# Optimization experiments

Hardware: AMD Instinct MI355X
Metric: run time of the kernel (lower is better)

## Reference

```python
import jax, jax.numpy as jnp
import numpy as np

V = 200      # v_dim
H = 400      # hidden
B, N = 1024, 128


def setup_inputs() -> dict:
    key = jax.random.key(0)
    ks = jax.random.split(key, 32)
    rn = lambda k, s, sc=0.05: jax.random.normal(k, s, dtype=jnp.float32) * sc
    merged = rn(ks[0], (B, N, 15), 1.0)
    # last column is the active flag in {0,1}; subject row (row 0) is active
    flag = jax.random.randint(ks[1], (B, N), 0, 2).astype(jnp.float32)
    flag = flag.at[:, 0].set(1.0)
    merged = merged.at[:, :, 14].set(flag)
    x = rn(ks[2], (B, N, 8), 1.0)
    a = rn(ks[3], (B,), 1.0)
    p = {
        # aug_attention = CrossAttentionLayer(7, 14, 200)
        'Wq_aug': rn(ks[4], (7, V)),  'bq_aug': rn(ks[5], (V,)),
        'Wk_aug': rn(ks[6], (14, V)), 'bk_aug': rn(ks[7], (V,)),
        'Wv_aug': rn(ks[8], (14, V)), 'bv_aug': rn(ks[9], (V,)),
        # o_attention = CrossAttentionLayer(7, 7, 200)
        'Wq_o': rn(ks[10], (7, V)),  'bq_o': rn(ks[11], (V,)),
        'Wk_o': rn(ks[12], (7, V)), 'bk_o': rn(ks[13], (V,)),
        'Wv_o': rn(ks[14], (7, V)), 'bv_o': rn(ks[15], (V,)),
        # shared BatchNorm1d(200)
        'bn_g': jnp.ones((V,), jnp.float32), 'bn_b': jnp.zeros((V,), jnp.float32),
        # six 200->200->1 ELU heads stacked: order [u,u_,d,d_,o,o_]
        'W3': rn(ks[16], (6, V, 200)), 'b3': rn(ks[17], (6, 200)),
        'W4': rn(ks[18], (6, 200)),    'b4': rn(ks[19], (6,)),
        # ego critic MLP 4->400->400->1
        'W0': rn(ks[20], (4, H)), 'b0': rn(ks[21], (H,)),
        'W1': rn(ks[22], (H, H)), 'b1': rn(ks[23], (H,)),
        'W2': rn(ks[24], (H, 1)), 'b2': rn(ks[25], (1,)),
    }
    return {'merged': merged, 'x': x, 'a': a, **p}


def _forward(merged, x, a, Wq_aug, bq_aug, Wk_aug, bk_aug, Wv_aug, bv_aug,
             Wq_o, bq_o, Wk_o, bk_o, Wv_o, bv_o, bn_g, bn_b,
             W3, b3, W4, b4, W0, b0, W1, b1, W2, b2):
    # --- event critic preprocessing (relative bus index) ---
    sub_bus = merged[:, 0, 0]
    merged = merged.at[:, :, 0].add(-sub_bus[:, None])
    merged = merged.at[:, :, 7].add(-sub_bus[:, None])
    sub_loc = merged[:, 0, 2][:, None]        # subject location
    flag = merged[:, :, 14]
    loc = merged[:, :, 2]
    u_mask = (loc < sub_loc) & (flag == 1.0)
    d_mask = (loc > sub_loc) & (flag == 1.0)
    f0 = flag == 0.0
    o_mask = f0 & (jnp.cumsum(f0.astype(jnp.int32), axis=1) > 1)  # drop first flag==0 row ([1:])
    ego7 = merged[:, 0, :7]                    # [B,7]
    scale = 1.0 / np.sqrt(float(V))

    def attend(Wq, bq, Wk, bk, Wv, bv, kv, masks):
        # variable-length cross-attention as masked softmax over padded keys
        q = ego7 @ Wq + bq                            # [B,V]
        k = jnp.einsum('bnf,fd->bnd', kv, Wk) + bk    # [B,N,V]
        v = jnp.einsum('bnf,fd->bnd', kv, Wv) + bv    # [B,N,V]
        s = jnp.einsum('bd,bnd->bn', q, k) * scale    # [B,N]
        outs = []
        for m in masks:
            w = jax.nn.softmax(jnp.where(m, s, -1e9), axis=1)
            o = jnp.einsum('bn,bnd->bd', w, v)
            outs.append(jnp.where(m.any(axis=1, keepdims=True), o, 0.0))
        return outs

    u_t, d_t = attend(Wq_aug, bq_aug, Wk_aug, bk_aug, Wv_aug, bv_aug,
                      merged[:, :, :14], [u_mask, d_mask])
    (o_t,) = attend(Wq_o, bq_o, Wk_o, bk_o, Wv_o, bv_o,
                    merged[:, :, :7], [o_mask])

    def bn(t):  # BatchNorm1d in training mode: per-call batch stats (biased var)
        m = t.mean(axis=0)
        var = t.var(axis=0)
        return bn_g * (t - m) / jnp.sqrt(var + 1e-5) + bn_b

    t = jnp.stack([bn(u_t), bn(d_t), bn(o_t)], axis=1)   # [B,3,V]
    th = t[:, jnp.array([0, 0, 1, 1, 2, 2])]             # [B,6,V] heads [u,u_,d,d_,o,o_]
    h = jax.nn.elu(jnp.einsum('bkf,kfg->bkg', th, W3) + b3)
    heads = jnp.einsum('bkg,kg->bk', h, W4) + b4         # [B,6]
    A1 = (heads[:, 0] + heads[:, 2] + heads[:, 4])[:, None]
    A2 = (heads[:, 1] + heads[:, 3] + heads[:, 5])[:, None]

    # --- ego critic ---
    ego4 = jnp.concatenate([x[:, 0, 4:7], a[:, None]], axis=1)  # cols [4,5,6], last <- a
    h1 = jax.nn.relu(ego4 @ W0 + b0)
    h1 = jax.nn.relu(h1 @ W1 + b1)
    Q1 = h1 @ W2 + b2                                    # [B,1]

    G1 = (Q1 + A1).reshape(-1, 1)
    G2 = (Q1 + A2).reshape(-1, 1)
    reg = jnp.zeros((1,), jnp.float32)
    return Q1, A2, G1, G2, reg


def reference(merged, x, a, Wq_aug, bq_aug, Wk_aug, bk_aug, Wv_aug, bv_aug,
              Wq_o, bq_o, Wk_o, bk_o, Wv_o, bv_o, bn_g, bn_b,
              W3, b3, W4, b4, W0, b0, W1, b1, W2, b2):
    return _forward(merged, x, a, Wq_aug, bq_aug, Wk_aug, bk_aug, Wv_aug, bv_aug,
                    Wq_o, bq_o, Wk_o, bk_o, Wv_o, bv_o, bn_g, bn_b,
                    W3, b3, W4, b4, W0, b0, W1, b1, W2, b2)
```

## Files before the change

kernel.cpp:

```cpp
#include <hip/hip_runtime.h>

#define BB 1024
#define NN 128
#define VV 200
#define HH 400

__device__ inline float wave_sum(float v){
  for (int o=32;o>0;o>>=1) v += __shfl_down(v,o);
  return v;
}
__device__ inline float xsum(float v){
  for (int o=1;o<64;o<<=1) v += __shfl_xor(v,o);
  return v;
}
__device__ inline float xmax(float v){
  for (int o=1;o<64;o<<=1) v = fmaxf(v,__shfl_xor(v,o));
  return v;
}

__global__ __launch_bounds__(64) void prep_k(
    const float* __restrict__ Wq_aug, const float* __restrict__ bq_aug,
    const float* __restrict__ Wk_aug, const float* __restrict__ bk_aug,
    const float* __restrict__ Wq_o,  const float* __restrict__ bq_o,
    const float* __restrict__ Wk_o,  const float* __restrict__ bk_o,
    float* __restrict__ prep)
{
  int t = blockIdx.x;
  int lane = threadIdx.x;
  const float *A, *Bv;
  if (t<98)      { int i=t/14, f=t-i*14; A=Wq_aug+i*VV; Bv=Wk_aug+f*VV; }
  else if (t<112){ int f=t-98;           A=bq_aug;      Bv=Wk_aug+f*VV; }
  else if (t<119){ int i=t-112;          A=Wq_aug+i*VV; Bv=bk_aug; }
  else if (t==119){                      A=bq_aug;      Bv=bk_aug; }
  else if (t<169){ int r=t-120; int i=r/7, f=r-i*7; A=Wq_o+i*VV; Bv=Wk_o+f*VV; }
  else if (t<176){ int f=t-169;          A=bq_o;        Bv=Wk_o+f*VV; }
  else if (t<183){ int i=t-176;          A=Wq_o+i*VV;   Bv=bk_o; }
  else           {                       A=bq_o;        Bv=bk_o; }
  float s=0;
  for (int d=lane; d<VV; d+=64) s += A[d]*Bv[d];
  s = xsum(s);
  if (lane==0) prep[t]=s;
}

__global__ __launch_bounds__(64) void attn_v2(
    const float* __restrict__ merged, const float* __restrict__ prep,
    const float* __restrict__ Wv_aug, const float* __restrict__ bv_aug,
    const float* __restrict__ Wv_o,  const float* __restrict__ bv_o,
    float* __restrict__ t_buf)
{
  const int b = blockIdx.x;
  const int lane = threadIdx.x;
  const float* base = merged + (size_t)b*NN*15;

  float sub_bus = base[0], sub_loc = base[2];
  float eg[7];
  eg[0]=0.0f;
  for (int i=1;i<7;i++) eg[i]=base[i];

  float wkqa[14], wkqo[7];
  #pragma unroll
  for (int f=0;f<14;f++){
    float s = prep[98+f];
    for (int i=1;i<7;i++) s += eg[i]*prep[i*14+f];
    wkqa[f]=s;
  }
  float qbka = prep[119];
  for (int i=1;i<7;i++) qbka += eg[i]*prep[112+i];
  #pragma unroll
  for (int f=0;f<7;f++){
    float s = prep[169+f];
    for (int i=1;i<7;i++) s += eg[i]*prep[120+i*7+f];
    wkqo[f]=s;
  }
  float qbko = prep[183];
  for (int i=1;i<7;i++) qbko += eg[i]*prep[176+i];

  float m0[15], m1[15];
  const float* r0 = base + (size_t)lane*15;
  const float* r1 = base + (size_t)(lane+64)*15;
  #pragma unroll
  for (int i=0;i<15;i++){ m0[i]=r0[i]; m1[i]=r1[i]; }
  m0[0]-=sub_bus; m0[7]-=sub_bus;
  m1[0]-=sub_bus; m1[7]-=sub_bus;

  const float scale = 0.07071067811865475f;
  float sa0=qbka, sa1=qbka, so0=qbko, so1=qbko;
  #pragma unroll
  for (int f=0;f<14;f++){ sa0+=m0[f]*wkqa[f]; sa1+=m1[f]*wkqa[f]; }
  #pragma unroll
  for (int f=0;f<7;f++){ so0+=m0[f]*wkqo[f]; so1+=m1[f]*wkqo[f]; }
  sa0*=scale; sa1*=scale; so0*=scale; so1*=scale;

  float fl0=m0[14], fl1=m1[14], lo0=m0[2], lo1=m1[2];
  bool um0=(lo0<sub_loc)&&(fl0==1.0f), um1=(lo1<sub_loc)&&(fl1==1.0f);
  bool dm0=(lo0>sub_loc)&&(fl0==1.0f), dm1=(lo1>sub_loc)&&(fl1==1.0f);
  bool f00=(fl0==0.0f), f01=(fl1==0.0f);
  unsigned long long bal0=__ballot(f00), bal1=__ballot(f01);
  unsigned long long below=(1ull<<lane)-1ull;
  int prior0=__popcll(bal0&below);
  int prior1=__popcll(bal0)+__popcll(bal1&below);
  bool om0=f00&&(prior0>0), om1=f01&&(prior1>0);

  const float NINF=-3.0e38f;
  float mu_ = xmax(fmaxf(um0?sa0:NINF, um1?sa1:NINF));
  bool anyu = mu_>-1e38f;
  float eu0 = um0?expf(sa0-mu_):0.0f, eu1 = um1?expf(sa1-mu_):0.0f;
  float su = xsum(eu0+eu1);
  float ivu = anyu?1.0f/su:0.0f;
  float wu0=eu0*ivu, wu1=eu1*ivu;
  float md_ = xmax(fmaxf(dm0?sa0:NINF, dm1?sa1:NINF));
  bool anyd = md_>-1e38f;
  float ed0 = dm0?expf(sa0-md_):0.0f, ed1 = dm1?expf(sa1-md_):0.0f;
  float sd = xsum(ed0+ed1);
  float ivd = anyd?1.0f/sd:0.0f;
  float wd0=ed0*ivd, wd1=ed1*ivd;
  float mo_ = xmax(fmaxf(om0?so0:NINF, om1?so1:NINF));
  bool anyo = mo_>-1e38f;
  float eo0 = om0?expf(so0-mo_):0.0f, eo1 = om1?expf(so1-mo_):0.0f;
  float so = xsum(eo0+eo1);
  float ivo = anyo?1.0f/so:0.0f;
  float wo0=eo0*ivo, wo1=eo1*ivo;

  float wfu[14], wfd[14], wfo[7];
  #pragma unroll
  for (int f=0;f<14;f++){
    wfu[f]=xsum(wu0*m0[f]+wu1*m1[f]);
    wfd[f]=xsum(wd0*m0[f]+wd1*m1[f]);
  }
  #pragma unroll
  for (int f=0;f<7;f++) wfo[f]=xsum(wo0*m0[f]+wo1*m1[f]);

  float* tb = t_buf + (size_t)b*600;
  #pragma unroll
  for (int rep=0;rep<4;rep++){
    int c = lane + rep*64;
    if (c < VV){
      float uv=bv_aug[c], dv=bv_aug[c], ov=bv_o[c];
      #pragma unroll
      for (int f=0;f<14;f++){
        float w=Wv_aug[f*VV+c];
        uv+=wfu[f]*w; dv+=wfd[f]*w;
      }
      #pragma unroll
      for (int f=0;f<7;f++) ov+=wfo[f]*Wv_o[f*VV+c];
      if(!anyu) uv=0.0f;
      if(!anyd) dv=0.0f;
      if(!anyo) ov=0.0f;
      tb[c]=uv; tb[200+c]=dv; tb[400+c]=ov;
    }
  }
}

__global__ __launch_bounds__(256) void bn_mlp(
    const float* __restrict__ t_buf,
    float* __restrict__ mean_out, float* __restrict__ rstd_out,
    const float* __restrict__ x, const float* __restrict__ a,
    const float* __restrict__ W0, const float* __restrict__ b0,
    const float* __restrict__ W1, const float* __restrict__ b1,
    const float* __restrict__ W2,
    float* __restrict__ mlp_part)
{
  int tid=threadIdx.x, wv=tid>>6, lane=tid&63;
  __shared__ float smem[8*HH + 4*64*9 + 64];

  if (blockIdx.x < 150){
    int c0 = blockIdx.x*4;
    float* ls  = smem;
    float* ls2 = smem+16;
    float s[4]={0,0,0,0}, s2[4]={0,0,0,0};
    #pragma unroll 2
    for (int b=tid;b<BB;b+=256){
      float4 v = *reinterpret_cast<const float4*>(t_buf + (size_t)b*600 + c0);
      s[0]+=v.x; s[1]+=v.y; s[2]+=v.z; s[3]+=v.w;
      s2[0]+=v.x*v.x; s2[1]+=v.y*v.y; s2[2]+=v.z*v.z; s2[3]+=v.w*v.w;
    }
    for (int c=0;c<4;c++){ s[c]=wave_sum(s[c]); s2[c]=wave_sum(s2[c]); }
    if (lane==0){
      for (int c=0;c<4;c++){ ls[wv*4+c]=s[c]; ls2[wv*4+c]=s2[c]; }
    }
    __syncthreads();
    if (tid<4){
      float S =ls[0*4+tid]+ls[1*4+tid]+ls[2*4+tid]+ls[3*4+tid];
      float S2=ls2[0*4+tid]+ls2[1*4+tid]+ls2[2*4+tid]+ls2[3*4+tid];
      float mean = S*(1.0f/BB);
      float var  = S2*(1.0f/BB) - mean*mean;
      mean_out[c0+tid]=mean;
      rstd_out[c0+tid]=rsqrtf(var+1e-5f);
    }
  } else {
    unsigned mu = blockIdx.x - 150;
    int js = mu >> 7;
    int xg = mu & 127;
    int bb = xg*8;
    float* h1s  = smem;
    float* part = smem + 8*HH;
    float* ego  = smem + 8*HH + 4*64*9;
    if (tid<32){
      int bl=tid>>2, j=tid&3;
      int b=bb+bl;
      ego[bl*4+j] = (j<3) ? x[(size_t)b*NN*8 + 4 + j] : a[b];
    }
    __syncthreads();
    for (int idx=tid; idx<8*HH; idx+=256){
      int bl = idx/HH, i = idx - bl*HH;
      float v = b0[i] + ego[bl*4+0]*W0[i]      + ego[bl*4+1]*W0[HH+i]
                      + ego[bl*4+2]*W0[2*HH+i] + ego[bl*4+3]*W0[3*HH+i];
      h1s[bl*HH+i] = fmaxf(v,0.0f);
    }
    __syncthreads();
    int jl = tid & 63;
    int ic = tid >> 6;
    int j  = js*64 + jl;
    bool jok = (j < HH);
    int jc = jok ? j : (HH-1);
    float acc[8]={0,0,0,0,0,0,0,0};
    {
      const float* w1p = W1 + jc;
      int i0 = ic*100;
      #pragma unroll 4
      for (int i=i0;i<i0+100;i++){
        float w = w1p[(size_t)i*HH];
        acc[0]+=h1s[0*HH+i]*w; acc[1]+=h1s[1*HH+i]*w;
        acc[2]+=h1s[2*HH+i]*w; acc[3]+=h1s[3*HH+i]*w;
        acc[4]+=h1s[4*HH+i]*w; acc[5]+=h1s[5*HH+i]*w;
        acc[6]+=h1s[6*HH+i]*w; acc[7]+=h1s[7*HH+i]*w;
      }
    }
    for (int bl=0;bl<8;bl++) part[(ic*64+jl)*9+bl]=acc[bl];
    __syncthreads();
    if (tid < 64){
      float bj = b1[jc], w2 = W2[jc];
      for (int bl=0;bl<8;bl++){
        float s = part[(0*64+jl)*9+bl]+part[(1*64+jl)*9+bl]
                + part[(2*64+jl)*9+bl]+part[(3*64+jl)*9+bl];
        s += bj;
        float contrib = jok ? fmaxf(s,0.0f)*w2 : 0.0f;
        float tot = wave_sum(contrib);
        if (jl==0) mlp_part[(size_t)(bb+bl)*8 + js] = tot;
      }
    }
  }
}

__global__ __launch_bounds__(256) void heads_k(
    const float* __restrict__ t_buf, const float* __restrict__ mean_in,
    const float* __restrict__ rstd_in,
    const float* __restrict__ bn_g, const float* __restrict__ bn_b,
    const float* __restrict__ W3, const float* __restrict__ b3,
    const float* __restrict__ W4, const float* __restrict__ b4,
    float* __restrict__ headv_ws)
{
  int bb = blockIdx.x*8;
  int k  = blockIdx.y;
  int tid=threadIdx.x, wv=tid>>6, lane=tid&63;
  int t3 = k>>1;
  __shared__ float tn[8][200];
  for (int idx=tid; idx<1600; idx+=256){
    int bl=idx/200, v=idx-bl*200;
    int c = t3*200+v;
    tn[bl][v] = bn_g[v]*(t_buf[(size_t)(bb+bl)*600+c]-mean_in[c])*rstd_in[c]+bn_b[v];
  }
  __syncthreads();
  float contrib[8]={0,0,0,0,0,0,0,0};
  int g = tid;
  if (g < 200){
    float acc[8];
    float bias = b3[k*200+g];
    for (int bl=0;bl<8;bl++) acc[bl]=bias;
    const float* w3p = W3 + (size_t)k*40000 + g;
    #pragma unroll 4
    for (int v=0;v<200;v++){
      float w = w3p[(size_t)v*200];
      acc[0]+=tn[0][v]*w; acc[1]+=tn[1][v]*w;
      acc[2]+=tn[2][v]*w; acc[3]+=tn[3][v]*w;
      acc[4]+=tn[4][v]*w; acc[5]+=tn[5][v]*w;
      acc[6]+=tn[6][v]*w; acc[7]+=tn[7][v]*w;
    }
    float w4 = W4[k*200+g];
    for (int bl=0;bl<8;bl++){
      float h = acc[bl]>0.f ? acc[bl] : (expf(acc[bl])-1.0f);
      contrib[bl] = h*w4;
    }
  }
  for (int bl=0;bl<8;bl++) contrib[bl]=wave_sum(contrib[bl]);
  __shared__ float red[4][8];
  if (lane==0) for (int bl=0;bl<8;bl++) red[wv][bl]=contrib[bl];
  __syncthreads();
  if (tid<8){
    float s = red[0][tid]+red[1][tid]+red[2][tid]+red[3][tid];
    headv_ws[(size_t)(bb+tid)*6 + k] = s + b4[k];
  }
}

__global__ __launch_bounds__(256) void finalize(
    const float* __restrict__ mlp_part, const float* __restrict__ headv_ws,
    const float* __restrict__ b2, float* __restrict__ out)
{
  int b = blockIdx.x*256 + threadIdx.x;
  if (b < BB){
    const float* mp = mlp_part + (size_t)b*8;
    float q = mp[0]+mp[1]+mp[2]+mp[3]+mp[4]+mp[5]+mp[6] + b2[0];
    const float* hv = headv_ws + (size_t)b*6;
    float A1 = hv[0]+hv[2]+hv[4];
    float A2 = hv[1]+hv[3]+hv[5];
    out[b]      = q;
    out[BB+b]   = A2;
    out[2*BB+b] = q+A1;
    out[3*BB+b] = q+A2;
    if (b==0) out[4*BB]=0.0f;
  }
}

extern "C" void kernel_launch(void* const* d_in, const int* in_sizes, int n_in,
                              void* d_out, int out_size, void* d_ws, size_t ws_size,
                              hipStream_t stream)
{
  (void)in_sizes; (void)n_in; (void)out_size; (void)ws_size;
  const float* merged=(const float*)d_in[0];
  const float* x     =(const float*)d_in[1];
  const float* a     =(const float*)d_in[2];
  const float* Wq_aug=(const float*)d_in[3];  const float* bq_aug=(const float*)d_in[4];
  const float* Wk_aug=(const float*)d_in[5];  const float* bk_aug=(const float*)d_in[6];
  const float* Wv_aug=(const float*)d_in[7];  const float* bv_aug=(const float*)d_in[8];
  const float* Wq_o  =(const float*)d_in[9];  const float* bq_o  =(const float*)d_in[10];
  const float* Wk_o  =(const float*)d_in[11]; const float* bk_o  =(const float*)d_in[12];
  const float* Wv_o  =(const float*)d_in[13]; const float* bv_o  =(const float*)d_in[14];
  const float* bn_g  =(const float*)d_in[15]; const float* bn_b  =(const float*)d_in[16];
  const float* W3    =(const float*)d_in[17]; const float* b3    =(const float*)d_in[18];
  const float* W4    =(const float*)d_in[19]; const float* b4    =(const float*)d_in[20];
  const float* W0    =(const float*)d_in[21]; const float* b0    =(const float*)d_in[22];
  const float* W1    =(const float*)d_in[23]; const float* b1    =(const float*)d_in[24];
  const float* W2    =(const float*)d_in[25]; const float* b2    =(const float*)d_in[26];

  float* out = (float*)d_out;
  float* ws  = (float*)d_ws;
  float* t_buf   = ws;
  float* mean_b  = ws + 614400;
  float* rstd_b  = ws + 615000;
  float* mlp_part= ws + 615600;
  float* headv_ws= ws + 623792;
  float* prep_b  = ws + 629936;

  hipLaunchKernelGGL(prep_k, dim3(184), dim3(64), 0, stream,
      Wq_aug,bq_aug,Wk_aug,bk_aug, Wq_o,bq_o,Wk_o,bk_o, prep_b);
  hipLaunchKernelGGL(attn_v2, dim3(BB), dim3(64), 0, stream,
      merged, prep_b, Wv_aug, bv_aug, Wv_o, bv_o, t_buf);
  hipLaunchKernelGGL(bn_mlp, dim3(150+896), dim3(256), 0, stream,
      t_buf, mean_b, rstd_b, x, a, W0, b0, W1, b1, W2, mlp_part);
  hipLaunchKernelGGL(heads_k, dim3(BB/8,6), dim3(256), 0, stream,
      t_buf, mean_b, rstd_b, bn_g, bn_b, W3, b3, W4, b4, headv_ws);
  hipLaunchKernelGGL(finalize, dim3(4), dim3(256), 0, stream,
      mlp_part, headv_ws, b2, out);
}
```

Measured before the change: 60.97 us.

## Fuse prep, attention, BN statistics and MLP into one front kernel

Merges the prep, attention and BN-stats/MLP kernels into a single `front` kernel. Each attention block now recomputes the 184 query-key dot products into shared memory and handles 4 batch rows, one per wave. Block-local channel sums and sums of squares are pushed into global fixed-point int64 atomics, which removes the separate BN reduction pass over t_buf. The heads kernel derives mean and rstd from those atomics and uses float4 shared-memory reads in its W3 loop. The change cuts kernel launches and one full read of t_buf, at the cost of a memset, atomic contention, redundant prep work per block and a small fixed-point quantisation of the statistics.

```diff
diff --git a/kernel.cpp b/kernel.cpp
--- a/kernel.cpp
+++ b/kernel.cpp
@@ -5,6 +5,9 @@
 #define VV 200
 #define HH 400
 
+#define S1F 268435456.0f
+#define S2F 67108864.0f
+
 __device__ inline float wave_sum(float v){
   for (int o=32;o>0;o>>=1) v += __shfl_down(v,o);
   return v;
@@ -18,177 +21,160 @@
   return v;
 }
 
-__global__ __launch_bounds__(64) void prep_k(
-    const float* __restrict__ Wq_aug, const float* __restrict__ bq_aug,
-    const float* __restrict__ Wk_aug, const float* __restrict__ bk_aug,
-    const float* __restrict__ Wq_o,  const float* __restrict__ bq_o,
-    const float* __restrict__ Wk_o,  const float* __restrict__ bk_o,
-    float* __restrict__ prep)
+struct FrontP {
+  const float *merged, *x, *a;
+  const float *Wq_aug,*bq_aug,*Wk_aug,*bk_aug,*Wv_aug,*bv_aug;
+  const float *Wq_o,*bq_o,*Wk_o,*bk_o,*Wv_o,*bv_o;
+  const float *W0,*b0,*W1,*b1,*W2;
+  float *t_buf, *mlp_part;
+  unsigned long long *ch_sum, *ch_sq;
+};
+
+__global__ __launch_bounds__(256,4) void front(FrontP p)
 {
-  int t = blockIdx.x;
-  int lane = threadIdx.x;
-  const float *A, *Bv;
-  if (t<98)      { int i=t/14, f=t-i*14; A=Wq_aug+i*VV; Bv=Wk_aug+f*VV; }
-  else if (t<112){ int f=t-98;           A=bq_aug;      Bv=Wk_aug+f*VV; }
-  else if (t<119){ int i=t-112;          A=Wq_aug+i*VV; Bv=bk_aug; }
-  else if (t==119){                      A=bq_aug;      Bv=bk_aug; }
-  else if (t<169){ int r=t-120; int i=r/7, f=r-i*7; A=Wq_o+i*VV; Bv=Wk_o+f*VV; }
-  else if (t<176){ int f=t-169;          A=bq_o;        Bv=Wk_o+f*VV; }
-  else if (t<183){ int i=t-176;          A=Wq_o+i*VV;   Bv=bk_o; }
-  else           {                       A=bq_o;        Bv=bk_o; }
-  float s=0;
-  for (int d=lane; d<VV; d+=64) s += A[d]*Bv[d];
-  s = xsum(s);
-  if (lane==0) prep[t]=s;
-}
-
-__global__ __launch_bounds__(64) void attn_v2(
-    const float* __restrict__ merged, const float* __restrict__ prep,
-    const float* __restrict__ Wv_aug, const float* __restrict__ bv_aug,
-    const float* __restrict__ Wv_o,  const float* __restrict__ bv_o,
-    float* __restrict__ t_buf)
-{
-  const int b = blockIdx.x;
-  const int lane = threadIdx.x;
-  const float* base = merged + (size_t)b*NN*15;
-
-  float sub_bus = base[0], sub_loc = base[2];
-  float eg[7];
-  eg[0]=0.0f;
-  for (int i=1;i<7;i++) eg[i]=base[i];
-
-  float wkqa[14], wkqo[7];
-  #pragma unroll
-  for (int f=0;f<14;f++){
-    float s = prep[98+f];
-    for (int i=1;i<7;i++) s += eg[i]*prep[i*14+f];
-    wkqa[f]=s;
-  }
-  float qbka = prep[119];
-  for (int i=1;i<7;i++) qbka += eg[i]*prep[112+i];
-  #pragma unroll
-  for (int f=0;f<7;f++){
-    float s = prep[169+f];
-    for (int i=1;i<7;i++) s += eg[i]*prep[120+i*7+f];
-    wkqo[f]=s;
-  }
-  float qbko = prep[183];
-  for (int i=1;i<7;i++) qbko += eg[i]*prep[176+i];
-
-  float m0[15], m1[15];
-  const float* r0 = base + (size_t)lane*15;
-  const float* r1 = base + (size_t)(lane+64)*15;
-  #pragma unroll
-  for (int i=0;i<15;i++){ m0[i]=r0[i]; m1[i]=r1[i]; }
-  m0[0]-=sub_bus; m0[7]-=sub_bus;
-  m1[0]-=sub_bus; m1[7]-=sub_bus;
-
-  const float scale = 0.07071067811865475f;
-  float sa0=qbka, sa1=qbka, so0=qbko, so1=qbko;
-  #pragma unroll
-  for (int f=0;f<14;f++){ sa0+=m0[f]*wkqa[f]; sa1+=m1[f]*wkqa[f]; }
-  #pragma unroll
-  for (int f=0;f<7;f++){ so0+=m0[f]*wkqo[f]; so1+=m1[f]*wkqo[f]; }
-  sa0*=scale; sa1*=scale; so0*=scale; so1*=scale;
-
-  float fl0=m0[14], fl1=m1[14], lo0=m0[2], lo1=m1[2];
-  bool um0=(lo0<sub_loc)&&(fl0==1.0f), um1=(lo1<sub_loc)&&(fl1==1.0f);
-  bool dm0=(lo0>sub_loc)&&(fl0==1.0f), dm1=(lo1>sub_loc)&&(fl1==1.0f);
-  bool f00=(fl0==0.0f), f01=(fl1==0.0f);
-  unsigned long long bal0=__ballot(f00), bal1=__ballot(f01);
-  unsigned long long below=(1ull<<lane)-1ull;
-  int prior0=__popcll(bal0&below);
-  int prior1=__popcll(bal0)+__popcll(bal1&below);
-  bool om0=f00&&(prior0>0), om1=f01&&(prior1>0);
-
-  const float NINF=-3.0e38f;
-  float mu_ = xmax(fmaxf(um0?sa0:NINF, um1?sa1:NINF));
-  bool anyu = mu_>-1e38f;
-  float eu0 = um0?expf(sa0-mu_):0.0f, eu1 = um1?expf(sa1-mu_):0.0f;
-  float su = xsum(eu0+eu1);
-  float ivu = anyu?1.0f/su:0.0f;
-  float wu0=eu0*ivu, wu1=eu1*ivu;
-  float md_ = xmax(fmaxf(dm0?sa0:NINF, dm1?sa1:NINF));
-  bool anyd = md_>-1e38f;
-  float ed0 = dm0?expf(sa0-md_):0.0f, ed1 = dm1?expf(sa1-md_):0.0f;
-  float sd = xsum(ed0+ed1);
-  float ivd = anyd?1.0f/sd:0.0f;
-  float wd0=ed0*ivd, wd1=ed1*ivd;
-  float mo_ = xmax(fmaxf(om0?so0:NINF, om1?so1:NINF));
-  bool anyo = mo_>-1e38f;
-  float eo0 = om0?expf(so0-mo_):0.0f, eo1 = om1?expf(so1-mo_):0.0f;
-  float so = xsum(eo0+eo1);
-  float ivo = anyo?1.0f/so:0.0f;
-  float wo0=eo0*ivo, wo1=eo1*ivo;
-
-  float wfu[14], wfd[14], wfo[7];
-  #pragma unroll
-  for (int f=0;f<14;f++){
-    wfu[f]=xsum(wu0*m0[f]+wu1*m1[f]);
-    wfd[f]=xsum(wd0*m0[f]+wd1*m1[f]);
-  }
-  #pragma unroll
-  for (int f=0;f<7;f++) wfo[f]=xsum(wo0*m0[f]+wo1*m1[f]);
-
-  float* tb = t_buf + (size_t)b*600;
-  #pragma unroll
-  for (int rep=0;rep<4;rep++){
-    int c = lane + rep*64;
-    if (c < VV){
-      float uv=bv_aug[c], dv=bv_aug[c], ov=bv_o[c];
-      #pragma unroll
-      for (int f=0;f<14;f++){
-        float w=Wv_aug[f*VV+c];
-        uv+=wfu[f]*w; dv+=wfd[f]*w;
+  const int tid = threadIdx.x;
+  const int wv = tid>>6, lane = tid&63;
+  __shared__ float smem[8*HH + 4*64*9 + 32];
+
+  if (blockIdx.x < 256){
+    float* prep_l = smem;
+    float* tred   = smem + 184;
+    const int bb = blockIdx.x*4;
+
+    for (int r=wv; r<184; r+=4){
+      const float *A, *Bv;
+      if (r<98)      { int i=r/14, f=r-i*14; A=p.Wq_aug+i*VV; Bv=p.Wk_aug+f*VV; }
+      else if (r<112){ int f=r-98;           A=p.bq_aug;      Bv=p.Wk_aug+f*VV; }
+      else if (r<119){ int i=r-112;          A=p.Wq_aug+i*VV; Bv=p.bk_aug; }
+      else if (r==119){                      A=p.bq_aug;      Bv=p.bk_aug; }
+      else if (r<169){ int q=r-120; int i=q/7, f=q-i*7; A=p.Wq_o+i*VV; Bv=p.Wk_o+f*VV; }
+      else if (r<176){ int f=r-169;          A=p.bq_o;        Bv=p.Wk_o+f*VV; }
+      else if (r<183){ int i=r-176;          A=p.Wq_o+i*VV;   Bv=p.bk_o; }
+      else           {                       A=p.bq_o;        Bv=p.bk_o; }
+      float s=0;
+      for (int d=lane; d<VV; d+=64) s += A[d]*Bv[d];
+      s = xsum(s);
+      if (lane==0) prep_l[r]=s;
+    }
+    __syncthreads();
+
+    const int b = bb + wv;
+    const float* base = p.merged + (size_t)b*NN*15;
+    float sub_bus = base[0], sub_loc = base[2];
+    float eg[7];
+    eg[0]=0.0f;
+    for (int i=1;i<7;i++) eg[i]=base[i];
+
+    float wkqa[14], wkqo[7];
+    #pragma unroll
+    for (int f=0;f<14;f++){
+      float s = prep_l[98+f];
+      for (int i=1;i<7;i++) s += eg[i]*prep_l[i*14+f];
+      wkqa[f]=s;
+    }
+    float qbka = prep_l[119];
+    for (int i=1;i<7;i++) qbka += eg[i]*prep_l[112+i];
+    #pragma unroll
+    for (int f=0;f<7;f++){
+      float s = prep_l[169+f];
+      for (int i=1;i<7;i++) s += eg[i]*prep_l[120+i*7+f];
+      wkqo[f]=s;
+    }
+    float qbko = prep_l[183];
+    for (int i=1;i<7;i++) qbko += eg[i]*prep_l[176+i];
+
+    float m0[15], m1[15];
+    const float* r0 = base + (size_t)lane*15;
+    const float* r1 = base + (size_t)(lane+64)*15;
+    #pragma unroll
+    for (int i=0;i<15;i++){ m0[i]=r0[i]; m1[i]=r1[i]; }
+    m0[0]-=sub_bus; m0[7]-=sub_bus;
+    m1[0]-=sub_bus; m1[7]-=sub_bus;
+
+    const float scale = 0.07071067811865475f;
+    float sa0=qbka, sa1=qbka, so0=qbko, so1=qbko;
+    #pragma unroll
+    for (int f=0;f<14;f++){ sa0+=m0[f]*wkqa[f]; sa1+=m1[f]*wkqa[f]; }
+    #pragma unroll
+    for (int f=0;f<7;f++){ so0+=m0[f]*wkqo[f]; so1+=m1[f]*wkqo[f]; }
+    sa0*=scale; sa1*=scale; so0*=scale; so1*=scale;
+
+    float fl0=m0[14], fl1=m1[14], lo0=m0[2], lo1=m1[2];
+    bool um0=(lo0<sub_loc)&&(fl0==1.0f), um1=(lo1<sub_loc)&&(fl1==1.0f);
+    bool dm0=(lo0>sub_loc)&&(fl0==1.0f), dm1=(lo1>sub_loc)&&(fl1==1.0f);
+    bool f00=(fl0==0.0f), f01=(fl1==0.0f);
+    unsigned long long bal0=__ballot(f00), bal1=__ballot(f01);
+    unsigned long long below=(1ull<<lane)-1ull;
+    int prior0=__popcll(bal0&below);
+    int prior1=__popcll(bal0)+__popcll(bal1&below);
+    bool om0=f00&&(prior0>0), om1=f01&&(prior1>0);
+
+    const float NINF=-3.0e38f;
+    float mu_ = xmax(fmaxf(um0?sa0:NINF, um1?sa1:NINF));
+    bool anyu = mu_>-1e38f;
+    float eu0 = um0?expf(sa0-mu_):0.0f, eu1 = um1?expf(sa1-mu_):0.0f;
+    float su = xsum(eu0+eu1);
+    float ivu = anyu?1.0f/su:0.0f;
+    float wu0=eu0*ivu, wu1=eu1*ivu;
+
+    float md_ = xmax(fmaxf(dm0?sa0:NINF, dm1?sa1:NINF));
+    bool anyd = md_>-1e38f;
+    float ed0 = dm0?expf(sa0-md_):0.0f, ed1 = dm1?expf(sa1-md_):0.0f;
+    float sd = xsum(ed0+ed1);
+    float ivd = anyd?1.0f/sd:0.0f;
+    float wd0=ed0*ivd, wd1=ed1*ivd;
+
+    float mo_ = xmax(fmaxf(om0?so0:NINF, om1?so1:NINF));
+    bool anyo = mo_>-1e38f;
+    float eo0 = om0?expf(so0-mo_):0.0f, eo1 = om1?expf(so1-mo_):0.0f;
+    float so = xsum(eo0+eo1);
+    float ivo = anyo?1.0f/so:0.0f;
+    float wo0=eo0*ivo, wo1=eo1*ivo;
+
+    float wfu[14], wfd[14], wfo[7];
+    #pragma unroll
+    for (int f=0;f<14;f++){
+      wfu[f]=xsum(wu0*m0[f]+wu1*m1[f]);
+      wfd[f]=xsum(wd0*m0[f]+wd1*m1[f]);
+    }
+    #pragma unroll
+    for (int f=0;f<7;f++) wfo[f]=xsum(wo0*m0[f]+wo1*m1[f]);
+
+    float* tb = p.t_buf + (size_t)b*600;
+    #pragma unroll
+    for (int rep=0;rep<4;rep++){
+      int c = lane + rep*64;
+      if (c < VV){
+        float uv=p.bv_aug[c], dv=p.bv_aug[c], ov=p.bv_o[c];
+        #pragma unroll
+        for (int f=0;f<14;f++){
+          float w=p.Wv_aug[f*VV+c];
+          uv+=wfu[f]*w; dv+=wfd[f]*w;
+        }
+        #pragma unroll
+        for (int f=0;f<7;f++) ov+=wfo[f]*p.Wv_o[f*VV+c];
+        if(!anyu) uv=0.0f;
+        if(!anyd) dv=0.0f;
+        if(!anyo) ov=0.0f;
+        tb[c]=uv; tb[200+c]=dv; tb[400+c]=ov;
+        tred[wv*600 + c]      = uv;
+        tred[wv*600 + 200+c]  = dv;
+        tred[wv*600 + 400+c]  = ov;
       }
-      #pragma unroll
-      for (int f=0;f<7;f++) ov+=wfo[f]*Wv_o[f*VV+c];
-      if(!anyu) uv=0.0f;
-      if(!anyd) dv=0.0f;
-      if(!anyo) ov=0.0f;
-      tb[c]=uv; tb[200+c]=dv; tb[400+c]=ov;
-    }
-  }
-}
-
-__global__ __launch_bounds__(256) void bn_mlp(
-    const float* __restrict__ t_buf,
-    float* __restrict__ mean_out, float* __restrict__ rstd_out,
-    const float* __restrict__ x, const float* __restrict__ a,
-    const float* __restrict__ W0, const float* __restrict__ b0,
-    const float* __restrict__ W1, const float* __restrict__ b1,
-    const float* __restrict__ W2,
-    float* __restrict__ mlp_part)
-{
-  int tid=threadIdx.x, wv=tid>>6, lane=tid&63;
-  __shared__ float smem[8*HH + 4*64*9 + 64];
-
-  if (blockIdx.x < 150){
-    int c0 = blockIdx.x*4;
-    float* ls  = smem;
-    float* ls2 = smem+16;
-    float s[4]={0,0,0,0}, s2[4]={0,0,0,0};
-    #pragma unroll 2
-    for (int b=tid;b<BB;b+=256){
-      float4 v = *reinterpret_cast<const float4*>(t_buf + (size_t)b*600 + c0);
-      s[0]+=v.x; s[1]+=v.y; s[2]+=v.z; s[3]+=v.w;
-      s2[0]+=v.x*v.x; s2[1]+=v.y*v.y; s2[2]+=v.z*v.z; s2[3]+=v.w*v.w;
-    }
-    for (int c=0;c<4;c++){ s[c]=wave_sum(s[c]); s2[c]=wave_sum(s2[c]); }
-    if (lane==0){
-      for (int c=0;c<4;c++){ ls[wv*4+c]=s[c]; ls2[wv*4+c]=s2[c]; }
-    }
-    __syncthreads();
-    if (tid<4){
-      float S =ls[0*4+tid]+ls[1*4+tid]+ls[2*4+tid]+ls[3*4+tid];
-      float S2=ls2[0*4+tid]+ls2[1*4+tid]+ls2[2*4+tid]+ls2[3*4+tid];
-      float mean = S*(1.0f/BB);
-      float var  = S2*(1.0f/BB) - mean*mean;
-      mean_out[c0+tid]=mean;
-      rstd_out[c0+tid]=rsqrtf(var+1e-5f);
+    }
+    __syncthreads();
+
+    for (int c=tid; c<600; c+=256){
+      float v0=tred[0*600+c], v1=tred[1*600+c], v2=tred[2*600+c], v3=tred[3*600+c];
+      float s  = (v0+v1)+(v2+v3);
+      float q  = (v0*v0+v1*v1)+(v2*v2+v3*v3);
+      unsigned long long us = (unsigned long long)(long long)llrintf(s*S1F);
+      unsigned long long uq = (unsigned long long)(long long)llrintf(q*S2F);
+      atomicAdd(p.ch_sum + c, us);
+      atomicAdd(p.ch_sq  + c, uq);
     }
   } else {
-    unsigned mu = blockIdx.x - 150;
+    unsigned mu = blockIdx.x - 256;
     int js = mu >> 7;
     int xg = mu & 127;
     int bb = xg*8;
@@ -198,13 +184,13 @@
     if (tid<32){
       int bl=tid>>2, j=tid&3;
       int b=bb+bl;
-      ego[bl*4+j] = (j<3) ? x[(size_t)b*NN*8 + 4 + j] : a[b];
+      ego[bl*4+j] = (j<3) ? p.x[(size_t)b*NN*8 + 4 + j] : p.a[b];
     }
     __syncthreads();
     for (int idx=tid; idx<8*HH; idx+=256){
       int bl = idx/HH, i = idx - bl*HH;
-      float v = b0[i] + ego[bl*4+0]*W0[i]      + ego[bl*4+1]*W0[HH+i]
-                      + ego[bl*4+2]*W0[2*HH+i] + ego[bl*4+3]*W0[3*HH+i];
+      float v = p.b0[i] + ego[bl*4+0]*p.W0[i]      + ego[bl*4+1]*p.W0[HH+i]
+                        + ego[bl*4+2]*p.W0[2*HH+i] + ego[bl*4+3]*p.W0[3*HH+i];
       h1s[bl*HH+i] = fmaxf(v,0.0f);
     }
     __syncthreads();
@@ -215,7 +201,7 @@
     int jc = jok ? j : (HH-1);
     float acc[8]={0,0,0,0,0,0,0,0};
     {
-      const float* w1p = W1 + jc;
+      const float* w1p = p.W1 + jc;
       int i0 = ic*100;
       #pragma unroll 4
       for (int i=i0;i<i0+100;i++){
@@ -229,22 +215,23 @@
     for (int bl=0;bl<8;bl++) part[(ic*64+jl)*9+bl]=acc[bl];
     __syncthreads();
     if (tid < 64){
-      float bj = b1[jc], w2 = W2[jc];
+      float bj = p.b1[jc], w2 = p.W2[jc];
       for (int bl=0;bl<8;bl++){
         float s = part[(0*64+jl)*9+bl]+part[(1*64+jl)*9+bl]
                 + part[(2*64+jl)*9+bl]+part[(3*64+jl)*9+bl];
         s += bj;
         float contrib = jok ? fmaxf(s,0.0f)*w2 : 0.0f;
         float tot = wave_sum(contrib);
-        if (jl==0) mlp_part[(size_t)(bb+bl)*8 + js] = tot;
+        if (jl==0) p.mlp_part[(size_t)(bb+bl)*8 + js] = tot;
       }
     }
   }
 }
 
-__global__ __launch_bounds__(256) void heads_k(
-    const float* __restrict__ t_buf, const float* __restrict__ mean_in,
-    const float* __restrict__ rstd_in,
+__global__ __launch_bounds__(256,4) void heads_k2(
+    const float* __restrict__ t_buf,
+    const unsigned long long* __restrict__ ch_sum,
+    const unsigned long long* __restrict__ ch_sq,
     const float* __restrict__ bn_g, const float* __restrict__ bn_b,
     const float* __restrict__ W3, const float* __restrict__ b3,
     const float* __restrict__ W4, const float* __restrict__ b4,
@@ -254,36 +241,61 @@
   int k  = blockIdx.y;
   int tid=threadIdx.x, wv=tid>>6, lane=tid&63;
   int t3 = k>>1;
+  __shared__ float mean_s[200], rstd_s[200];
   __shared__ float tn[8][200];
+  __shared__ float red[4][8];
+
+  for (int c=tid; c<200; c+=256){
+    int ch = t3*200+c;
+    long long is = (long long)ch_sum[ch];
+    long long iq = (long long)ch_sq[ch];
+    float S = (float)is * (1.0f/S1F);
+    float Q = (float)iq * (1.0f/S2F);
+    float mean = S*(1.0f/BB);
+    float var  = Q*(1.0f/BB) - mean*mean;
+    mean_s[c]=mean;
+    rstd_s[c]=rsqrtf(var+1e-5f);
+  }
+  __syncthreads();
+
   for (int idx=tid; idx<1600; idx+=256){
     int bl=idx/200, v=idx-bl*200;
-    int c = t3*200+v;
-    tn[bl][v] = bn_g[v]*(t_buf[(size_t)(bb+bl)*600+c]-mean_in[c])*rstd_in[c]+bn_b[v];
+    float t = t_buf[(size_t)(bb+bl)*600 + t3*200 + v];
+    tn[bl][v] = bn_g[v]*(t-mean_s[v])*rstd_s[v]+bn_b[v];
   }
   __syncthreads();
-  float contrib[8]={0,0,0,0,0,0,0,0};
+
   int g = tid;
-  if (g < 200){
-    float acc[8];
-    float bias = b3[k*200+g];
+  int gc = (g<200)? g : 199;
+  float acc[8];
+  {
+    float bias = b3[k*200+gc];
     for (int bl=0;bl<8;bl++) acc[bl]=bias;
-    const float* w3p = W3 + (size_t)k*40000 + g;
-    #pragma unroll 4
-    for (int v=0;v<200;v++){
-      float w = w3p[(size_t)v*200];
-      acc[0]+=tn[0][v]*w; acc[1]+=tn[1][v]*w;
-      acc[2]+=tn[2][v]*w; acc[3]+=tn[3][v]*w;
-      acc[4]+=tn[4][v]*w; acc[5]+=tn[5][v]*w;
-      acc[6]+=tn[6][v]*w; acc[7]+=tn[7][v]*w;
-    }
-    float w4 = W4[k*200+g];
+  }
+  const float* w3p = W3 + (size_t)k*40000 + gc;
+  const float4* tn4 = reinterpret_cast<const float4*>(&tn[0][0]);
+  #pragma unroll 2
+  for (int v4=0; v4<50; v4++){
+    int v = v4*4;
+    float w0 = w3p[(size_t)v*200];
+    float w1 = w3p[(size_t)(v+1)*200];
+    float w2 = w3p[(size_t)(v+2)*200];
+    float w3v= w3p[(size_t)(v+3)*200];
+    #pragma unroll
     for (int bl=0;bl<8;bl++){
-      float h = acc[bl]>0.f ? acc[bl] : (expf(acc[bl])-1.0f);
-      contrib[bl] = h*w4;
-    }
-  }
+      float4 t = tn4[bl*50+v4];
+      acc[bl] += t.x*w0 + t.y*w1 + t.z*w2 + t.w*w3v;
+    }
+  }
+  float w4 = W4[k*200+gc];
+  float contrib[8];
+  #pragma unroll
+  for (int bl=0;bl<8;bl++){
+    float h = acc[bl]>0.f ? acc[bl] : (expf(acc[bl])-1.0f);
+    contrib[bl] = (g<200) ? h*w4 : 0.0f;
+  }
+  #pragma unroll
   for (int bl=0;bl<8;bl++) contrib[bl]=wave_sum(contrib[bl]);
-  __shared__ float red[4][8];
   if (lane==0) for (int bl=0;bl<8;bl++) red[wv][bl]=contrib[bl];
   __syncthreads();
   if (tid<8){
@@ -316,39 +328,40 @@
                               hipStream_t stream)
 {
   (void)in_sizes; (void)n_in; (void)out_size; (void)ws_size;
-  const float* merged=(const float*)d_in[0];
-  const float* x     =(const float*)d_in[1];
-  const float* a     =(const float*)d_in[2];
-  const float* Wq_aug=(const float*)d_in[3];  const float* bq_aug=(const float*)d_in[4];
-  const float* Wk_aug=(const float*)d_in[5];  const float* bk_aug=(const float*)d_in[6];
-  const float* Wv_aug=(const float*)d_in[7];  const float* bv_aug=(const float*)d_in[8];
-  const float* Wq_o  =(const float*)d_in[9];  const float* bq_o  =(const float*)d_in[10];
-  const float* Wk_o  =(const float*)d_in[11]; const float* bk_o  =(const float*)d_in[12];
-  const float* Wv_o  =(const float*)d_in[13]; const float* bv_o  =(const float*)d_in[14];
-  const float* bn_g  =(const float*)d_in[15]; const float* bn_b  =(const float*)d_in[16];
-  const float* W3    =(const float*)d_in[17]; const float* b3    =(const float*)d_in[18];
-  const float* W4    =(const float*)d_in[19]; const float* b4    =(const float*)d_in[20];
-  const float* W0    =(const float*)d_in[21]; const float* b0    =(const float*)d_in[22];
-  const float* W1    =(const float*)d_in[23]; const float* b1    =(const float*)d_in[24];
-  const float* W2    =(const float*)d_in[25]; const float* b2    =(const float*)d_in[26];
-
+  float* ws  = (float*)d_ws;
   float* out = (float*)d_out;
-  float* ws  = (float*)d_ws;
-  float* t_buf   = ws;
-  float* mean_b  = ws + 614400;
-  float* rstd_b  = ws + 615000;
-  float* mlp_part= ws + 615600;
-  float* headv_ws= ws + 623792;
-  float* prep_b  = ws + 629936;
-
-  hipLaunchKernelGGL(prep_k, dim3(184), dim3(64), 0, stream,
-      Wq_aug,bq_aug,Wk_aug,bk_aug, Wq_o,bq_o,Wk_o,bk_o, prep_b);
-  hipLaunchKernelGGL(attn_v2, dim3(BB), dim3(64), 0, stream,
-      merged, prep_b, Wv_aug, bv_aug, Wv_o, bv_o, t_buf);
-  hipLaunchKernelGGL(bn_mlp, dim3(150+896), dim3(256), 0, stream,
-      t_buf, mean_b, rstd_b, x, a, W0, b0, W1, b1, W2, mlp_part);
-  hipLaunchKernelGGL(heads_k, dim3(BB/8,6), dim3(256), 0, stream,
-      t_buf, mean_b, rstd_b, bn_g, bn_b, W3, b3, W4, b4, headv_ws);
+
+  FrontP P;
+  P.merged=(const float*)d_in[0];
+  P.x     =(const float*)d_in[1];
+  P.a     =(const float*)d_in[2];
+  P.Wq_aug=(const float*)d_in[3];  P.bq_aug=(const float*)d_in[4];
+  P.Wk_aug=(const float*)d_in[5];  P.bk_aug=(const float*)d_in[6];
+  P.Wv_aug=(const float*)d_in[7];  P.bv_aug=(const float*)d_in[8];
+  P.Wq_o  =(const float*)d_in[9];  P.bq_o  =(const float*)d_in[10];
+  P.Wk_o  =(const float*)d_in[11]; P.bk_o  =(const float*)d_in[12];
+  P.Wv_o  =(const float*)d_in[13]; P.bv_o  =(const float*)d_in[14];
+  P.W0    =(const float*)d_in[21]; P.b0    =(const float*)d_in[22];
+  P.W1    =(const float*)d_in[23]; P.b1    =(const float*)d_in[24];
+  P.W2    =(const float*)d_in[25];
+  const float* bn_g =(const float*)d_in[15];
+  const float* bn_b =(const float*)d_in[16];
+  const float* W3   =(const float*)d_in[17];
+  const float* b3   =(const float*)d_in[18];
+  const float* W4   =(const float*)d_in[19];
+  const float* b4   =(const float*)d_in[20];
+  const float* b2   =(const float*)d_in[26];
+
+  P.t_buf   = ws;
+  P.mlp_part= ws + 615600;
+  float* headv_ws = ws + 623792;
+  P.ch_sum = (unsigned long long*)(ws + 632000);
+  P.ch_sq  = (unsigned long long*)(ws + 633200);
+
+  hipMemsetAsync((void*)P.ch_sum, 0, 2*600*sizeof(unsigned long long), stream);
+  hipLaunchKernelGGL(front, dim3(256+896), dim3(256), 0, stream, P);
+  hipLaunchKernelGGL(heads_k2, dim3(BB/8,6), dim3(256), 0, stream,
+      P.t_buf, P.ch_sum, P.ch_sq, bn_g, bn_b, W3, b3, W4, b4, headv_ws);
   hipLaunchKernelGGL(finalize, dim3(4), dim3(256), 0, stream,
-      mlp_part, headv_ws, b2, out);
-}
+      P.mlp_part, headv_ws, b2, out);
+}
```

After: 76.56 us. 25.6% more time.

## Fuse prep into attention and finalize into heads via completion counter

Applied to the files above, without the earlier changes.

Removes the separate prep kernel: each 256-thread attention block recomputes the 184 query-key weight dot products into shared memory, then handles four batch rows, one per wave. The finalize kernel is folded into the heads kernel through a per-row-group atomic counter, so the last of the six head blocks writes the outputs. A memset is added to reset the counters. The heads inner loop now reads shared memory as float4. This trades two kernel launches for redundant prep work in every attention block plus an extra memset and atomics.

```diff
diff --git a/kernel.cpp b/kernel.cpp
--- a/kernel.cpp
+++ b/kernel.cpp
@@ -18,40 +18,40 @@
   return v;
 }
 
-__global__ __launch_bounds__(64) void prep_k(
+__global__ __launch_bounds__(256) void k_attn(
+    const float* __restrict__ merged,
     const float* __restrict__ Wq_aug, const float* __restrict__ bq_aug,
     const float* __restrict__ Wk_aug, const float* __restrict__ bk_aug,
+    const float* __restrict__ Wv_aug, const float* __restrict__ bv_aug,
     const float* __restrict__ Wq_o,  const float* __restrict__ bq_o,
     const float* __restrict__ Wk_o,  const float* __restrict__ bk_o,
-    float* __restrict__ prep)
-{
-  int t = blockIdx.x;
-  int lane = threadIdx.x;
-  const float *A, *Bv;
-  if (t<98)      { int i=t/14, f=t-i*14; A=Wq_aug+i*VV; Bv=Wk_aug+f*VV; }
-  else if (t<112){ int f=t-98;           A=bq_aug;      Bv=Wk_aug+f*VV; }
-  else if (t<119){ int i=t-112;          A=Wq_aug+i*VV; Bv=bk_aug; }
-  else if (t==119){                      A=bq_aug;      Bv=bk_aug; }
-  else if (t<169){ int r=t-120; int i=r/7, f=r-i*7; A=Wq_o+i*VV; Bv=Wk_o+f*VV; }
-  else if (t<176){ int f=t-169;          A=bq_o;        Bv=Wk_o+f*VV; }
-  else if (t<183){ int i=t-176;          A=Wq_o+i*VV;   Bv=bk_o; }
-  else           {                       A=bq_o;        Bv=bk_o; }
-  float s=0;
-  for (int d=lane; d<VV; d+=64) s += A[d]*Bv[d];
-  s = xsum(s);
-  if (lane==0) prep[t]=s;
-}
-
-__global__ __launch_bounds__(64) void attn_v2(
-    const float* __restrict__ merged, const float* __restrict__ prep,
-    const float* __restrict__ Wv_aug, const float* __restrict__ bv_aug,
     const float* __restrict__ Wv_o,  const float* __restrict__ bv_o,
     float* __restrict__ t_buf)
 {
-  const int b = blockIdx.x;
-  const int lane = threadIdx.x;
+  const int tid = threadIdx.x;
+  const int wv = tid>>6, lane = tid&63;
+  __shared__ float prep_l[184];
+  const int bb = blockIdx.x*4;
+
+  for (int r=wv; r<184; r+=4){
+    const float *A, *Bv;
+    if (r<98)      { int i=r/14, f=r-i*14; A=Wq_aug+i*VV; Bv=Wk_aug+f*VV; }
+    else if (r<112){ int f=r-98;           A=bq_aug;      Bv=Wk_aug+f*VV; }
+    else if (r<119){ int i=r-112;          A=Wq_aug+i*VV; Bv=bk_aug; }
+    else if (r==119){                      A=bq_aug;      Bv=bk_aug; }
+    else if (r<169){ int q=r-120; int i=q/7, f=q-i*7; A=Wq_o+i*VV; Bv=Wk_o+f*VV; }
+    else if (r<176){ int f=r-169;          A=bq_o;        Bv=Wk_o+f*VV; }
+    else if (r<183){ int i=r-176;          A=Wq_o+i*VV;   Bv=bk_o; }
+    else           {                       A=bq_o;        Bv=bk_o; }
+    float s=0;
+    for (int d=lane; d<VV; d+=64) s += A[d]*Bv[d];
+    s = xsum(s);
+    if (lane==0) prep_l[r]=s;
+  }
+  __syncthreads();
+
+  const int b = bb + wv;
   const float* base = merged + (size_t)b*NN*15;
-
   float sub_bus = base[0], sub_loc = base[2];
   float eg[7];
   eg[0]=0.0f;
@@ -60,20 +60,20 @@
   float wkqa[14], wkqo[7];
   #pragma unroll
   for (int f=0;f<14;f++){
-    float s = prep[98+f];
-    for (int i=1;i<7;i++) s += eg[i]*prep[i*14+f];
+    float s = prep_l[98+f];
+    for (int i=1;i<7;i++) s += eg[i]*prep_l[i*14+f];
     wkqa[f]=s;
   }
-  float qbka = prep[119];
-  for (int i=1;i<7;i++) qbka += eg[i]*prep[112+i];
+  float qbka = prep_l[119];
+  for (int i=1;i<7;i++) qbka += eg[i]*prep_l[112+i];
   #pragma unroll
   for (int f=0;f<7;f++){
-    float s = prep[169+f];
-    for (int i=1;i<7;i++) s += eg[i]*prep[120+i*7+f];
+    float s = prep_l[169+f];
+    for (int i=1;i<7;i++) s += eg[i]*prep_l[120+i*7+f];
     wkqo[f]=s;
   }
-  float qbko = prep[183];
-  for (int i=1;i<7;i++) qbko += eg[i]*prep[176+i];
+  float qbko = prep_l[183];
+  for (int i=1;i<7;i++) qbko += eg[i]*prep_l[176+i];
 
   float m0[15], m1[15];
   const float* r0 = base + (size_t)lane*15;
@@ -108,12 +108,14 @@
   float su = xsum(eu0+eu1);
   float ivu = anyu?1.0f/su:0.0f;
   float wu0=eu0*ivu, wu1=eu1*ivu;
+
   float md_ = xmax(fmaxf(dm0?sa0:NINF, dm1?sa1:NINF));
   bool anyd = md_>-1e38f;
   float ed0 = dm0?expf(sa0-md_):0.0f, ed1 = dm1?expf(sa1-md_):0.0f;
   float sd = xsum(ed0+ed1);
   float ivd = anyd?1.0f/sd:0.0f;
   float wd0=ed0*ivd, wd1=ed1*ivd;
+
   float mo_ = xmax(fmaxf(om0?so0:NINF, om1?so1:NINF));
   bool anyo = mo_>-1e38f;
   float eo0 = om0?expf(so0-mo_):0.0f, eo1 = om1?expf(so1-mo_):0.0f;
@@ -151,7 +153,7 @@
   }
 }
 
-__global__ __launch_bounds__(256) void bn_mlp(
+__global__ __launch_bounds__(256) void k_mlpbn(
     const float* __restrict__ t_buf,
     float* __restrict__ mean_out, float* __restrict__ rstd_out,
     const float* __restrict__ x, const float* __restrict__ a,
@@ -242,72 +244,93 @@
   }
 }
 
-__global__ __launch_bounds__(256) void heads_k(
+__global__ __launch_bounds__(256) void k_headsfin(
     const float* __restrict__ t_buf, const float* __restrict__ mean_in,
     const float* __restrict__ rstd_in,
     const float* __restrict__ bn_g, const float* __restrict__ bn_b,
     const float* __restrict__ W3, const float* __restrict__ b3,
     const float* __restrict__ W4, const float* __restrict__ b4,
-    float* __restrict__ headv_ws)
+    const float* __restrict__ mlp_part, const float* __restrict__ b2,
+    float* __restrict__ headv_ws, unsigned* __restrict__ done_cnt,
+    float* __restrict__ out)
 {
   int bb = blockIdx.x*8;
   int k  = blockIdx.y;
   int tid=threadIdx.x, wv=tid>>6, lane=tid&63;
   int t3 = k>>1;
   __shared__ float tn[8][200];
+  __shared__ float red[4][8];
+  __shared__ unsigned oldc;
+
   for (int idx=tid; idx<1600; idx+=256){
     int bl=idx/200, v=idx-bl*200;
     int c = t3*200+v;
     tn[bl][v] = bn_g[v]*(t_buf[(size_t)(bb+bl)*600+c]-mean_in[c])*rstd_in[c]+bn_b[v];
   }
   __syncthreads();
-  float contrib[8]={0,0,0,0,0,0,0,0};
+
   int g = tid;
-  if (g < 200){
-    float acc[8];
-    float bias = b3[k*200+g];
+  int gc = (g<200)? g : 199;
+  bool act = (g<200);
+  float acc[8];
+  {
+    float bias = b3[k*200+gc];
     for (int bl=0;bl<8;bl++) acc[bl]=bias;
-    const float* w3p = W3 + (size_t)k*40000 + g;
-    #pragma unroll 4
-    for (int v=0;v<200;v++){
-      float w = w3p[(size_t)v*200];
-      acc[0]+=tn[0][v]*w; acc[1]+=tn[1][v]*w;
-      acc[2]+=tn[2][v]*w; acc[3]+=tn[3][v]*w;
-      acc[4]+=tn[4][v]*w; acc[5]+=tn[5][v]*w;
-      acc[6]+=tn[6][v]*w; acc[7]+=tn[7][v]*w;
-    }
-    float w4 = W4[k*200+g];
+  }
+  const float* w3p = W3 + (size_t)k*40000 + gc;
+  const float4* tn4 = reinterpret_cast<const float4*>(&tn[0][0]);
+  #pragma unroll 2
+  for (int v4=0; v4<50; v4++){
+    int v = v4*4;
+    float w0 = w3p[(size_t)v*200];
+    float w1 = w3p[(size_t)(v+1)*200];
+    float w2 = w3p[(size_t)(v+2)*200];
+    float w3v= w3p[(size_t)(v+3)*200];
+    #pragma unroll
     for (int bl=0;bl<8;bl++){
-      float h = acc[bl]>0.f ? acc[bl] : (expf(acc[bl])-1.0f);
-      contrib[bl] = h*w4;
-    }
-  }
+      float4 t = tn4[bl*50+v4];
+      acc[bl] += t.x*w0 + t.y*w1 + t.z*w2 + t.w*w3v;
+    }
+  }
+  float w4 = W4[k*200+gc];
+  float contrib[8];
+  #pragma unroll
+  for (int bl=0;bl<8;bl++){
+    float h = acc[bl]>0.f ? acc[bl] : (expf(acc[bl])-1.0f);
+    contrib[bl] = act ? h*w4 : 0.0f;
+  }
+  #pragma unroll
   for (int bl=0;bl<8;bl++) contrib[bl]=wave_sum(contrib[bl]);
-  __shared__ float red[4][8];
   if (lane==0) for (int bl=0;bl<8;bl++) red[wv][bl]=contrib[bl];
   __syncthreads();
   if (tid<8){
     float s = red[0][tid]+red[1][tid]+red[2][tid]+red[3][tid];
     headv_ws[(size_t)(bb+tid)*6 + k] = s + b4[k];
-  }
-}
-
-__global__ __launch_bounds__(256) void finalize(
-    const float* __restrict__ mlp_part, const float* __restrict__ headv_ws,
-    const float* __restrict__ b2, float* __restrict__ out)
-{
-  int b = blockIdx.x*256 + threadIdx.x;
-  if (b < BB){
-    const float* mp = mlp_part + (size_t)b*8;
-    float q = mp[0]+mp[1]+mp[2]+mp[3]+mp[4]+mp[5]+mp[6] + b2[0];
-    const float* hv = headv_ws + (size_t)b*6;
-    float A1 = hv[0]+hv[2]+hv[4];
-    float A2 = hv[1]+hv[3]+hv[5];
-    out[b]      = q;
-    out[BB+b]   = A2;
-    out[2*BB+b] = q+A1;
-    out[3*BB+b] = q+A2;
-    if (b==0) out[4*BB]=0.0f;
+    __threadfence();
+  }
+  __syncthreads();
+
+  if (tid==0){
+    __threadfence();
+    oldc = atomicAdd(done_cnt + blockIdx.x, 1u);
+  }
+  __syncthreads();
+
+  if (oldc == 5u){
+    __threadfence();
+    if (tid < 8){
+      int b = bb + tid;
+      const float* hv = headv_ws + (size_t)b*6;
+      float A1 = hv[0]+hv[2]+hv[4];
+      float A2 = hv[1]+hv[3]+hv[5];
+      const float* mp = mlp_part + (size_t)b*8;
+      float q = mp[0]+mp[1]+mp[2]+mp[3]+mp[4]+mp[5]+mp[6] + b2[0];
+      out[b]      = q;
+      out[BB+b]   = A2;
+      out[2*BB+b] = q+A1;
+      out[3*BB+b] = q+A2;
+    }
+    if (blockIdx.x==0 && tid==8) out[4*BB]=0.0f;
   }
 }
 
@@ -316,6 +339,9 @@
                               hipStream_t stream)
 {
   (void)in_sizes; (void)n_in; (void)out_size; (void)ws_size;
+  float* ws  = (float*)d_ws;
+  float* out = (float*)d_out;
+
   const float* merged=(const float*)d_in[0];
   const float* x     =(const float*)d_in[1];
   const float* a     =(const float*)d_in[2];
@@ -332,23 +358,20 @@
   const float* W1    =(const float*)d_in[23]; const float* b1    =(const float*)d_in[24];
   const float* W2    =(const float*)d_in[25]; const float* b2    =(const float*)d_in[26];
 
-  float* out = (float*)d_out;
-  float* ws  = (float*)d_ws;
-  float* t_buf   = ws;
-  float* mean_b  = ws + 614400;
-  float* rstd_b  = ws + 615000;
-  float* mlp_part= ws + 615600;
-  float* headv_ws= ws + 623792;
-  float* prep_b  = ws + 629936;
-
-  hipLaunchKernelGGL(prep_k, dim3(184), dim3(64), 0, stream,
-      Wq_aug,bq_aug,Wk_aug,bk_aug, Wq_o,bq_o,Wk_o,bk_o, prep_b);
-  hipLaunchKernelGGL(attn_v2, dim3(BB), dim3(64), 0, stream,
-      merged, prep_b, Wv_aug, bv_aug, Wv_o, bv_o, t_buf);
-  hipLaunchKernelGGL(bn_mlp, dim3(150+896), dim3(256), 0, stream,
+  float* t_buf    = ws;
+  float* mean_b   = ws + 614400;
+  float* rstd_b   = ws + 615000;
+  float* mlp_part = ws + 615600;
+  float* headv_ws = ws + 623792;
+  unsigned* done  = (unsigned*)(ws + 629936);
+
+  hipMemsetAsync((void*)done, 0, 128*sizeof(unsigned), stream);
+  hipLaunchKernelGGL(k_attn, dim3(256), dim3(256), 0, stream, merged,
+      Wq_aug,bq_aug,Wk_aug,bk_aug,Wv_aug,bv_aug,
+      Wq_o,bq_o,Wk_o,bk_o,Wv_o,bv_o, t_buf);
+  hipLaunchKernelGGL(k_mlpbn, dim3(150+896), dim3(256), 0, stream,
       t_buf, mean_b, rstd_b, x, a, W0, b0, W1, b1, W2, mlp_part);
-  hipLaunchKernelGGL(heads_k, dim3(BB/8,6), dim3(256), 0, stream,
-      t_buf, mean_b, rstd_b, bn_g, bn_b, W3, b3, W4, b4, headv_ws);
-  hipLaunchKernelGGL(finalize, dim3(4), dim3(256), 0, stream,
-      mlp_part, headv_ws, b2, out);
-}
+  hipLaunchKernelGGL(k_headsfin, dim3(128,6), dim3(256), 0, stream,
+      t_buf, mean_b, rstd_b, bn_g, bn_b, W3, b3, W4, b4,
+      mlp_part, b2, headv_ws, done, out);
+}
```

Result: slower. 127.2 us (+108.7%).
